# Kernel tuning notes

Hardware: AMD Instinct MI355X
Metric: run time of the kernel (lower is better)

The kernel has to match this reference:

```python
import jax, jax.numpy as jnp
import numpy as np
from jax import lax

# STE sign: forward maps x>=0 -> +1, x<0 -> -1 (matches XORQuantizeSTE)
@jax.custom_vjp
def ste_sign(x):
    return jnp.where(x >= 0, jnp.ones_like(x), -jnp.ones_like(x))

def _ste_fwd(x):
    return ste_sign(x), None

def _ste_bwd(_, g):
    return (g,)  # identity pass-through

ste_sign.defvjp(_ste_fwd, _ste_bwd)


def _xor_quant(x, w):
    """Per-layer XNOR-Net quantization: alpha = mean|W| scales both
    binarized activation and binarized weight (as in the wrapper's hook
    + binarization())."""
    alpha = jnp.mean(jnp.abs(w))
    return alpha * ste_sign(x), alpha * ste_sign(w)


def _conv(x, w, b, stride):
    y = lax.conv_general_dilated(
        x, w, window_strides=(stride, stride), padding=((1, 1), (1, 1)),
        dimension_numbers=('NCHW', 'OIHW', 'NCHW'))
    return y + b[None, :, None, None]


def setup_inputs() -> dict:
    key = jax.random.key(0)
    ks = jax.random.split(key, 9)
    f32 = jnp.float32
    x = jax.random.normal(ks[0], (32, 3, 224, 224), dtype=f32)
    w1 = jax.random.normal(ks[1], (64, 3, 3, 3), dtype=f32) * 0.1
    b1 = jax.random.normal(ks[2], (64,), dtype=f32) * 0.01
    w2 = jax.random.normal(ks[3], (128, 64, 3, 3), dtype=f32) * 0.05
    b2 = jax.random.normal(ks[4], (128,), dtype=f32) * 0.01
    w3 = jax.random.normal(ks[5], (256, 128, 3, 3), dtype=f32) * 0.03
    b3 = jax.random.normal(ks[6], (256,), dtype=f32) * 0.01
    wf = jax.random.normal(ks[7], (1000, 256), dtype=f32) * 0.05
    bf = jax.random.normal(ks[8], (1000,), dtype=f32) * 0.01
    return {'x': x, 'w1': w1, 'b1': b1, 'w2': w2, 'b2': b2,
            'w3': w3, 'b3': b3, 'wf': wf, 'bf': bf}


def reference(x, w1, b1, w2, b2, w3, b3, wf, bf):
    # layer 1: binarize activation + weight with shared alpha, dense conv
    xq, wq = _xor_quant(x, w1)
    h = jnp.clip(_conv(xq, wq, b1, 2), -1.0, 1.0)   # [32,64,112,112]
    xq, wq = _xor_quant(h, w2)
    h = jnp.clip(_conv(xq, wq, b2, 2), -1.0, 1.0)   # [32,128,56,56]
    xq, wq = _xor_quant(h, w3)
    h = jnp.clip(_conv(xq, wq, b3, 2), -1.0, 1.0)   # [32,256,28,28]
    h = jnp.mean(h, axis=(2, 3))                     # global avg pool [32,256]
    xq, wq = _xor_quant(h, wf)
    return xq @ wq.T + bf                            # [32,1000]
```

## Files before the change

### kernel.cpp

```cpp
#include <hip/hip_runtime.h>
#include <stdint.h>
#include <math.h>


#define WP2_OFF    2048ull
#define WP3T_OFF   16384ull
#define WFP_OFF    65536ull
#define PART_OFF   100352ull
#define P1_OFF     102400ull
#define P2_OFF     3313664ull
#define POOLP_OFF  4919296ull

__global__ __launch_bounds__(256) void k1_conv1_pack(
    const float* __restrict__ x,  const float* __restrict__ w1, const float* __restrict__ b1,
    const float* __restrict__ w2, const float* __restrict__ w3, const float* __restrict__ wf,
    uint64_t* __restrict__ wp2, uint64_t* __restrict__ wp3t, uint64_t* __restrict__ wfp,
    double* __restrict__ part, uint64_t* __restrict__ p1)
{
    const int tid = threadIdx.x, lane = tid & 63, wid = tid >> 6, bid = blockIdx.x;
    if (bid < 1568) {
        __shared__ double a2s;
        __shared__ uint32_t wm[64];
        __shared__ int Ts[64];
        if (wid == 0) {
            double s = 0.0;
            #pragma unroll
            for (int i = 0; i < 27; i++) s += fabs((double)w1[lane + i*64]);
            #pragma unroll
            for (int off = 1; off < 64; off <<= 1) s += __shfl_xor(s, off, 64);
            if (lane == 0) { double a = s / 1728.0; a2s = a * a; }
        } else if (wid == 1) {
            uint32_t m = 0;
            for (int t = 0; t < 27; t++) {
                int ci = t / 9, r = t % 9, kh = r / 3, kw = r % 3;
                if (w1[((lane*3 + ci)*3 + kh)*3 + kw] >= 0.f) m |= (1u << t);
            }
            wm[lane] = m;
        }
        int idx = bid * 256 + tid;
        int wo = idx % 112, t1 = idx / 112;
        int ho = t1 % 112, n = t1 / 112;
        uint32_t xm = 0, vm = 0;
        #pragma unroll
        for (int ci = 0; ci < 3; ci++)
            #pragma unroll
            for (int kh = 0; kh < 3; kh++) {
                int hi = 2*ho + kh - 1;
                if ((unsigned)hi >= 224u) continue;
                #pragma unroll
                for (int kw = 0; kw < 3; kw++) {
                    int wi = 2*wo + kw - 1;
                    if ((unsigned)wi >= 224u) continue;
                    int t = ci*9 + kh*3 + kw;
                    vm |= (1u << t);
                    if (x[((n*3 + ci)*224 + hi)*224 + wi] >= 0.f) xm |= (1u << t);
                }
            }
        __syncthreads();
        if (tid < 64) {
            double a2 = a2s, b = (double)b1[tid];
            int k = (int)ceil(-b / a2);
            k = max(-27, min(28, k));
            while (k > -27 && (a2 * (double)(k - 1) + b >= 0.0)) k--;
            while (k <= 27 && !(a2 * (double)k + b >= 0.0)) k++;
            Ts[tid] = k;
        }
        __syncthreads();
        int V = __popc(vm);
        uint64_t bits = 0;
        for (int co = 0; co < 64; co++) {
            int m = __popc((~(xm ^ wm[co])) & vm);
            if (2*m - V >= Ts[co]) bits |= (1ull << co);
        }
        p1[idx] = bits;
    } else {
        int rel = bid - 1568;
        if (rel < 96) {
            __shared__ double sd[256];
            int t = rel >> 5, c = rel & 31;
            const float* w; int n;
            if (t == 0)      { w = w2; n = 128*64*9; }
            else if (t == 1) { w = w3; n = 256*128*9; }
            else             { w = wf; n = 1000*256; }
            int per = (n + 31) / 32;
            int lo = c * per, hi = min(n, lo + per);
            double s0 = 0.0, s1 = 0.0, s2 = 0.0, s3 = 0.0;
            int i = lo + tid;
            for (; i + 768 < hi; i += 1024) {
                s0 += fabs((double)w[i]);
                s1 += fabs((double)w[i + 256]);
                s2 += fabs((double)w[i + 512]);
                s3 += fabs((double)w[i + 768]);
            }
            for (; i < hi; i += 256) s0 += fabs((double)w[i]);
            sd[tid] = (s0 + s1) + (s2 + s3);
            __syncthreads();
            for (int off = 128; off > 0; off >>= 1) {
                if (tid < off) sd[tid] += sd[tid + off];
                __syncthreads();
            }
            if (tid == 0) part[(t + 1)*32 + c] = sd[0];
        }
        int gw = rel * 4 + wid;
        const int nw = 640;
        for (int w = gw; w < 1152; w += nw) {
            int co = w / 9, tap = w % 9, kh = tap / 3, kw = tap % 3;
            uint64_t b = __ballot(w2[((co*64 + lane)*3 + kh)*3 + kw] >= 0.f);
            if (lane == 0) wp2[w] = b;
        }
        for (int w = gw; w < 4608; w += nw) {
            int co = w / 18, r = w % 18, tap = r / 2, half = r & 1;
            int kh = tap / 3, kw = tap % 3;
            uint64_t b = __ballot(w3[((co*128 + half*64 + lane)*3 + kh)*3 + kw] >= 0.f);
            if (lane == 0) wp3t[(tap*2 + half)*256 + co] = b;
        }
        for (int w = gw; w < 4000; w += nw) {
            int o = w >> 2, j = w & 3;
            uint64_t b = __ballot(wf[o*256 + j*64 + lane] >= 0.f);
            if (lane == 0) wfp[w] = b;
        }
    }
}

__global__ __launch_bounds__(256) void k2_conv2(
    const uint64_t* __restrict__ p1, const float* __restrict__ b2,
    const double* __restrict__ part, const uint64_t* __restrict__ wp2g,
    uint32_t* __restrict__ p2)
{
    __shared__ uint64_t wp[1152];
    __shared__ uint64_t xs[1152];
    __shared__ int      M[128*4];
    const int tid = threadIdx.x, lane = tid & 63;

    for (int i = tid; i < 1152; i += 256) wp[i] = wp2g[i];
    for (int i = tid; i < 1152; i += 256) {
        int t = i >> 7, pl = i & 127;
        int pos = blockIdx.x * 128 + pl;
        int wo = pos % 56, t1 = pos / 56;
        int ho = t1 % 56, n = t1 / 56;
        int kh = t / 3, kw = t % 3;
        int hi = 2*ho + kh - 1, wi = 2*wo + kw - 1;
        bool ok = ((unsigned)hi < 112u) && ((unsigned)wi < 112u);
        xs[i] = ok ? p1[(n*112 + hi)*112 + wi] : 0ull;
    }
    __syncthreads();
    if (tid < 128) {
        int co = tid;
        double s = 0.0;
        for (int j = 0; j < 32; j++) s += part[32 + j];
        double a = s / (double)(128*64*9);
        double a2 = a * a, b = (double)b2[co];
        int k = (int)ceil(-b / a2);
        k = max(-577, min(578, k));
        while (k > -577 && (a2 * (double)(k - 1) + b >= 0.0)) k--;
        while (k <= 577 && !(a2 * (double)k + b >= 0.0)) k++;
        uint32_t P[9];
        #pragma unroll
        for (int t = 0; t < 9; t++) P[t] = __popcll(wp[co*9 + t]);
        int cT = P[0] + P[1] + P[2];
        int cL = P[0] + P[3] + P[6];
        int cC = P[0];
        #pragma unroll
        for (int cfg = 0; cfg < 4; cfg++) {
            int isT = cfg & 1, isL = (cfg >> 1) & 1;
            int V = 9 - 3*isT - 3*isL + (isT & isL);
            int corr = isT*cT + isL*cL - (isT & isL)*cC;
            int dtab = 64*V + 2*corr;
            M[co*4 + cfg] = (dtab - k) >> 1;
        }
    }
    __syncthreads();

    int q = tid >> 6;
    int co0 = q * 32;
    int pos0 = blockIdx.x * 128 + lane;
    int pos1 = pos0 + 64;
    int wo0 = pos0 % 56, ho0 = (pos0 / 56) % 56;
    int wo1 = pos1 % 56, ho1 = (pos1 / 56) % 56;
    int cfg0 = (ho0 == 0 ? 1 : 0) | (wo0 == 0 ? 2 : 0);
    int cfg1 = (ho1 == 0 ? 1 : 0) | (wo1 == 0 ? 2 : 0);
    uint64_t xv0[9], xv1[9];
    #pragma unroll
    for (int t = 0; t < 9; t++) { xv0[t] = xs[t*128 + lane]; xv1[t] = xs[t*128 + 64 + lane]; }
    uint32_t bits0 = 0, bits1 = 0;
    for (int c = 0; c < 32; c++) {
        int co = co0 + c;
        int mm0 = 0, mm1 = 0;
        #pragma unroll
        for (int t = 0; t < 9; t++) {
            uint64_t w = wp[co*9 + t];
            mm0 += __popcll(xv0[t] ^ w);
            mm1 += __popcll(xv1[t] ^ w);
        }
        if (mm0 <= M[co*4 + cfg0]) bits0 |= (1u << c);
        if (mm1 <= M[co*4 + cfg1]) bits1 |= (1u << c);
    }
    p2[pos0*4 + q] = bits0;
    p2[pos1*4 + q] = bits1;
}

__global__ __launch_bounds__(256) void k3_conv3pool(
    const uint64_t* __restrict__ p2, const float* __restrict__ b3,
    const double* __restrict__ part, const uint64_t* __restrict__ wp3t,
    double* __restrict__ partial)
{
    __shared__ uint64_t xs[28*18];
    const int tid = threadIdx.x;
    int n = blockIdx.x / 28, ho = blockIdx.x % 28;

    double s = 0.0;
    for (int j = 0; j < 32; j++) s += part[64 + j];
    double a = s / (double)(256*128*9);
    double a2 = a * a;

    uint64_t w[18];
    #pragma unroll
    for (int i = 0; i < 18; i++) w[i] = wp3t[i*256 + tid];
    uint32_t P[9];
    #pragma unroll
    for (int t = 0; t < 9; t++) P[t] = __popcll(w[2*t]) + __popcll(w[2*t+1]);

    for (int i = tid; i < 504; i += 256) {
        int wo = i / 18, r = i % 18;
        int tap = r / 2, half = r % 2;
        int kh = tap / 3, kw = tap % 3;
        int hi = 2*ho + kh - 1, wi = 2*wo + kw - 1;
        bool ok = ((unsigned)hi < 56u) && ((unsigned)wi < 56u);
        xs[i] = ok ? p2[(size_t)((n*56 + hi)*56 + wi)*2 + half] : 0ull;
    }
    __syncthreads();

    bool htop = (ho == 0);
    int rv = htop ? 2 : 3;
    double bc = (double)b3[tid];
    double sum = 0.0;
    for (int wo = 0; wo < 28; wo++) {
        int mm = 0;
        #pragma unroll
        for (int t = 0; t < 18; t++)
            mm += __popcll(xs[wo*18 + t] ^ w[t]);
        bool wl = (wo == 0);
        int cv = wl ? 2 : 3;
        int corr = 0;
        if (htop) corr += P[0] + P[1] + P[2];
        if (wl)   corr += P[0] + P[3] + P[6];
        if (htop && wl) corr -= P[0];
        int dot = 128*(rv*cv) - 2*mm + 2*corr;
        double h = a2 * (double)dot + bc;
        h = fmin(fmax(h, -1.0), 1.0);
        sum += h;
    }
    partial[(size_t)(n*28 + ho)*256 + tid] = sum;
}

__global__ __launch_bounds__(256) void k4_poolfc(
    const double* __restrict__ partial, const uint64_t* __restrict__ wfp,
    const float* __restrict__ bf, const double* __restrict__ part,
    float* __restrict__ out)
{
    __shared__ uint64_t spl[4];
    const int tid = threadIdx.x, lane = tid & 63;
    int n = blockIdx.x;
    double s = 0.0;
    for (int c = 0; c < 28; c++) s += partial[(size_t)(n*28 + c)*256 + tid];
    uint64_t bal = __ballot((s / 784.0) >= 0.0);
    if (lane == 0) spl[tid >> 6] = bal;

    double sa = 0.0;
    for (int j = 0; j < 32; j++) sa += part[96 + j];
    double a = sa / (double)(1000*256);
    double aa = a * a;
    __syncthreads();
    uint64_t s0 = spl[0], s1 = spl[1], s2 = spl[2], s3 = spl[3];
    for (int o = tid; o < 1000; o += 256) {
        int m = __popcll(s0 ^ wfp[o*4]) + __popcll(s1 ^ wfp[o*4+1])
              + __popcll(s2 ^ wfp[o*4+2]) + __popcll(s3 ^ wfp[o*4+3]);
        out[n*1000 + o] = (float)(aa * (double)(256 - 2*m) + (double)bf[o]);
    }
}

extern "C" void kernel_launch(void* const* d_in, const int* in_sizes, int n_in,
                              void* d_out, int out_size, void* d_ws, size_t ws_size,
                              hipStream_t stream) {
    const float* x  = (const float*)d_in[0];
    const float* w1 = (const float*)d_in[1];
    const float* b1 = (const float*)d_in[2];
    const float* w2 = (const float*)d_in[3];
    const float* b2 = (const float*)d_in[4];
    const float* w3 = (const float*)d_in[5];
    const float* b3 = (const float*)d_in[6];
    const float* wf = (const float*)d_in[7];
    const float* bf = (const float*)d_in[8];

    char* ws = (char*)d_ws;
    uint64_t* wp2    = (uint64_t*)(ws + WP2_OFF);
    uint64_t* wp3t   = (uint64_t*)(ws + WP3T_OFF);
    uint64_t* wfp    = (uint64_t*)(ws + WFP_OFF);
    double*   part   = (double*)  (ws + PART_OFF);
    uint64_t* p1     = (uint64_t*)(ws + P1_OFF);
    uint32_t* p2     = (uint32_t*)(ws + P2_OFF);
    double*   poolp  = (double*)  (ws + POOLP_OFF);
    float*    out    = (float*)   d_out;

    hipLaunchKernelGGL(k1_conv1_pack, dim3(1728), dim3(256), 0, stream,
                       x, w1, b1, w2, w3, wf, wp2, wp3t, wfp, part, p1);
    hipLaunchKernelGGL(k2_conv2,      dim3(784),  dim3(256), 0, stream,
                       p1, b2, part, wp2, p2);
    hipLaunchKernelGGL(k3_conv3pool,  dim3(896),  dim3(256), 0, stream,
                       (const uint64_t*)p2, b3, part, wp3t, poolp);
    hipLaunchKernelGGL(k4_poolfc,     dim3(32),   dim3(256), 0, stream,
                       poolp, wfp, bf, part, out);
}
```

Baseline: 146.0 us.

## Tile conv1 by output row strips with shared-memory input staging and bit packing

Each conv1 block now covers four output rows of one image instead of 256 scattered output pixels. It loads the needed input rows into LDS as coalesced float4 reads and packs their signs into 32-bit words, then each thread builds its 27-bit window by shifting those words. This replaces the strided, uncoalesced per-thread global loads of 27 input floats and cuts redundant reads of overlapping windows. The cost is a larger LDS footprint, extra barriers, and more complicated boundary-masking logic.

```diff
diff --git a/kernel.cpp b/kernel.cpp
--- a/kernel.cpp
+++ b/kernel.cpp
@@ -18,10 +18,18 @@
     double* __restrict__ part, uint64_t* __restrict__ p1)
 {
     const int tid = threadIdx.x, lane = tid & 63, wid = tid >> 6, bid = blockIdx.x;
-    if (bid < 1568) {
-        __shared__ double a2s;
+    if (bid < 896) {
+        __shared__ float4   xf4[1512];
+        __shared__ uint32_t xb[216];
         __shared__ uint32_t wm[64];
-        __shared__ int Ts[64];
+        __shared__ int      Ts[64];
+        __shared__ double   a2s;
+        const float* xf = (const float*)xf4;
+
+        int n = bid / 28, hb = bid % 28;
+        int ho0 = hb * 4;
+        int hi0 = 2 * ho0 - 1;
+
         if (wid == 0) {
             double s = 0.0;
             #pragma unroll
@@ -37,25 +45,15 @@
             }
             wm[lane] = m;
         }
-        int idx = bid * 256 + tid;
-        int wo = idx % 112, t1 = idx / 112;
-        int ho = t1 % 112, n = t1 / 112;
-        uint32_t xm = 0, vm = 0;
-        #pragma unroll
-        for (int ci = 0; ci < 3; ci++)
-            #pragma unroll
-            for (int kh = 0; kh < 3; kh++) {
-                int hi = 2*ho + kh - 1;
-                if ((unsigned)hi >= 224u) continue;
-                #pragma unroll
-                for (int kw = 0; kw < 3; kw++) {
-                    int wi = 2*wo + kw - 1;
-                    if ((unsigned)wi >= 224u) continue;
-                    int t = ci*9 + kh*3 + kw;
-                    vm |= (1u << t);
-                    if (x[((n*3 + ci)*224 + hi)*224 + wi] >= 0.f) xm |= (1u << t);
-                }
-            }
+        const float4* xg = (const float4*)x;
+        for (int i = tid; i < 1512; i += 256) {
+            int seg = i / 56, f4 = i % 56;
+            int ci = seg / 9, r = seg % 9;
+            int hi = hi0 + r;
+            float4 v = make_float4(0.f, 0.f, 0.f, 0.f);
+            if ((unsigned)hi < 224u) v = xg[((n*3 + ci)*224 + hi)*56 + f4];
+            xf4[i] = v;
+        }
         __syncthreads();
         if (tid < 64) {
             double a2 = a2s, b = (double)b1[tid];
@@ -65,16 +63,60 @@
             while (k <= 27 && !(a2 * (double)k + b >= 0.0)) k++;
             Ts[tid] = k;
         }
+        if (tid < 189) {
+            int seg = tid / 7, j = tid % 7;
+            uint32_t u = 0;
+            #pragma unroll
+            for (int k = 0; k < 32; k++) {
+                int o = (k + tid) & 31;
+                if (xf[seg*224 + j*32 + o] >= 0.f) u |= (1u << o);
+            }
+            xb[seg*8 + j] = u;
+        } else if (tid < 216) {
+            xb[(tid - 189)*8 + 7] = 0u;
+        }
         __syncthreads();
-        int V = __popc(vm);
-        uint64_t bits = 0;
-        for (int co = 0; co < 64; co++) {
-            int m = __popc((~(xm ^ wm[co])) & vm);
-            if (2*m - V >= Ts[co]) bits |= (1ull << co);
-        }
-        p1[idx] = bits;
+
+        for (int pass = 0; pass < 2; pass++) {
+            int s = tid + pass*256;
+            if (s >= 448) break;
+            int dho = s / 112, wo = s % 112;
+            int hop = ho0 + dho;
+            uint32_t vm = 0x7FFFFFFu;
+            if (hop == 0) vm &= ~0x1C0E07u;
+            if (wo == 0)  vm &= ~0x1249249u;
+            int c0 = 2*wo - 1;
+            uint32_t xm = 0;
+            if (wo > 0) {
+                int w0 = c0 >> 5, sh = c0 & 31;
+                #pragma unroll
+                for (int ci = 0; ci < 3; ci++)
+                    #pragma unroll
+                    for (int kh = 0; kh < 3; kh++) {
+                        int seg = ci*9 + 2*dho + kh;
+                        uint64_t dw = (uint64_t)xb[seg*8 + w0]
+                                    | ((uint64_t)xb[seg*8 + w0 + 1] << 32);
+                        xm |= (uint32_t)((dw >> sh) & 7u) << (ci*9 + kh*3);
+                    }
+            } else {
+                #pragma unroll
+                for (int ci = 0; ci < 3; ci++)
+                    #pragma unroll
+                    for (int kh = 0; kh < 3; kh++) {
+                        int seg = ci*9 + 2*dho + kh;
+                        xm |= ((xb[seg*8] << 1) & 6u) << (ci*9 + kh*3);
+                    }
+            }
+            int V = __popc(vm);
+            uint64_t bits = 0;
+            for (int co = 0; co < 64; co++) {
+                int m = __popc((~(xm ^ wm[co])) & vm);
+                if (2*m - V >= Ts[co]) bits |= (1ull << co);
+            }
+            p1[(n*112 + hop)*112 + wo] = bits;
+        }
     } else {
-        int rel = bid - 1568;
+        int rel = bid - 896;
         if (rel < 96) {
             __shared__ double sd[256];
             int t = rel >> 5, c = rel & 31;
@@ -302,7 +344,7 @@
     double*   poolp  = (double*)  (ws + POOLP_OFF);
     float*    out    = (float*)   d_out;
 
-    hipLaunchKernelGGL(k1_conv1_pack, dim3(1728), dim3(256), 0, stream,
+    hipLaunchKernelGGL(k1_conv1_pack, dim3(1056), dim3(256), 0, stream,
                        x, w1, b1, w2, w3, wf, wp2, wp3t, wfp, part, p1);
     hipLaunchKernelGGL(k2_conv2,      dim3(784),  dim3(256), 0, stream,
                        p1, b2, part, wp2, p2);
```

After: 142.8 us. 2.1% less time.
